# Kernel tuning notes

Measured on AMD Instinct MI355X. Metric: run time of the kernel, lower is better.

The kernel has to match this reference:

```python
import jax, jax.numpy as jnp
import numpy as np

B, SST, SL = 16, 256, 48
VOCAB, D, CH = 16384, 64, 112
TPI = 0.0


def setup_inputs() -> dict:
    key = jax.random.key(0)
    ks = jax.random.split(key, 26)
    def n(k, shp, s=0.05):
        return jax.random.normal(k, shp, dtype=jnp.float32) * s
    return {
        "x": jax.random.randint(ks[0], (B, SST), 0, VOCAB),
        "ees": n(ks[1], (B, D, SL), 1.0),
        "emb": n(ks[2], (VOCAB, D)),
        "cl0_w": n(ks[3], (CH, D, 1)),  "cl0_b": n(ks[4], (CH,)),
        "cl1_w": n(ks[5], (CH, CH, 3)), "cl1_b": n(ks[6], (CH,)),
        "claa_w": n(ks[7], (CH, CH, 3)), "claa_b": n(ks[8], (CH,)),
        "clfa_w": n(ks[9], (CH, CH, 3)), "clfa_b": n(ks[10], (CH,)),
        "ccac_w": n(ks[11], (CH, CH, 3)), "ccac_b": n(ks[12], (CH,)),
        "cib_w": n(ks[13], (D, CH, 1)),  "cib_b": n(ks[14], (D,)),
        "cpr1_w": n(ks[15], (D, 2 * D, 1)), "cpr1_b": n(ks[16], (D,)),
        "cpr2_w": n(ks[17], (D, D, 1)),  "cpr2_b": n(ks[18], (D,)),
        "cma_w": n(ks[19], (CH, D, 1)),  "cma_b": n(ks[20], (CH,)),
        "ccf_w": n(ks[21], (D, CH, 1)),  "ccf_b": n(ks[22], (D,)),
        "fff_b": n(ks[23], (VOCAB,)),
    }


def _conv1x1(x, w, b):
    # x: [B,C,S], w: [O,C,1] -> [B,O,S]
    return jnp.einsum('oc,bcs->bos', w[:, :, 0], x) + b[None, :, None]


def _conv3(x, w, b):
    # valid 1D conv, channels-first. x: [B,C,S+2] -> [B,O,S]
    y = jax.lax.conv_general_dilated(x, w, (1,), 'VALID',
                                     dimension_numbers=('NCH', 'OIH', 'NCH'))
    return y + b[None, :, None]


def _forward(x, ees, emb, cl0_w, cl0_b, cl1_w, cl1_b, claa_w, claa_b,
             clfa_w, clfa_b, ccac_w, ccac_b, cib_w, cib_b,
             cpr1_w, cpr1_b, cpr2_w, cpr2_b, cma_w, cma_b,
             ccf_w, ccf_b, fff_b):
    b = x.shape[0]
    pre_d = jnp.transpose(emb[x], (0, 2, 1))            # [B,64,SST]
    t = _conv1x1(pre_d, cl0_w, cl0_b)                   # [B,112,SST]
    tp = jnp.full((b, CH, 2), TPI, dtype=t.dtype)       # tpi pad columns

    # split cpr layer1 weight into the t-half and ees-half (concat along ch)
    wt, we = cpr1_w[:, :D, 0], cpr1_w[:, D:, 0]

    def stage(t_in, conv_w, conv_b):
        tt = jnp.concatenate([tp, t_in], axis=2)        # [B,112,SST+2]
        xconv = jax.nn.relu(_conv3(tt, conv_w, conv_b))  # [B,112,SST]
        c = _conv1x1(xconv, cib_w, cib_b)               # [B,64,SST]
        # all-pairs broadcast (sl x sst) + 1x1-conv MLP, equivalent to
        # repeat/concat/cpr in the original, without duplicating data
        h = (jnp.einsum('oc,bcs->bos', wt, c)[:, :, None, :]
             + jnp.einsum('oc,bcl->bol', we, ees)[:, :, :, None]
             + cpr1_b[None, :, None, None])             # [B,64,SL,SST]
        h = jax.nn.relu(h)
        h = jax.nn.relu(jnp.einsum('oc,bcls->bols', cpr2_w[:, :, 0], h)
                        + cpr2_b[None, :, None, None])
        m = jnp.max(h, axis=2)                          # max over sl -> [B,64,SST]
        return _conv1x1(m, cma_w, cma_b) + xconv        # residual add

    t = stage(t, cl1_w, cl1_b)
    t = stage(t, claa_w, claa_b)
    t = stage(t, clfa_w, clfa_b)
    t = stage(t, ccac_w, ccac_b)

    ccf_out = _conv1x1(t, ccf_w, ccf_b)                 # [B,64,SST]
    # tied-weight output projection: [B,SST,64] @ emb.T -> [B,SST,VOCAB]
    output = jnp.einsum('bds,vd->bsv', ccf_out, emb) + fff_b
    return output, pre_d, ccf_out


def reference(x, ees, emb, cl0_w, cl0_b, cl1_w, cl1_b, claa_w, claa_b,
              clfa_w, clfa_b, ccac_w, ccac_b, cib_w, cib_b,
              cpr1_w, cpr1_b, cpr2_w, cpr2_b, cma_w, cma_b,
              ccf_w, ccf_b, fff_b):
    return _forward(x, ees, emb, cl0_w, cl0_b, cl1_w, cl1_b, claa_w, claa_b,
                    clfa_w, clfa_b, ccac_w, ccac_b, cib_w, cib_b,
                    cpr1_w, cpr1_b, cpr2_w, cpr2_b, cma_w, cma_b,
                    ccf_w, ccf_b, fff_b)
```

## Files before the change

### kernel.cpp

```cpp
#include <hip/hip_runtime.h>

#define B_ 16
#define SST 256
#define SL 48
#define VOCAB 16384
#define D_ 64
#define CH 112

#define OUT0_ELEMS ((size_t)B_*SST*VOCAB)
#define OUT1_ELEMS (B_*D_*SST)

typedef __attribute__((ext_vector_type(8))) short s8v;
typedef __attribute__((ext_vector_type(4))) float f32x4;

#define MFMA(a,b,c) __builtin_amdgcn_mfma_f32_16x16x32_bf16(a, b, c, 0, 0, 0)

__device__ __forceinline__ void split1(float f, unsigned short* h, unsigned short* l) {
    unsigned u = __float_as_uint(f);
    *h = (unsigned short)(u >> 16);
    float lo = f - __uint_as_float(u & 0xffff0000u);
    *l = (unsigned short)(__float_as_uint(lo) >> 16);
}
__device__ __forceinline__ uint2 split_pack2(float f0, float f1) {
    unsigned u0 = __float_as_uint(f0), u1 = __float_as_uint(f1);
    unsigned hp = (u0 >> 16) | (u1 & 0xffff0000u);
    float l0 = f0 - __uint_as_float(u0 & 0xffff0000u);
    float l1 = f1 - __uint_as_float(u1 & 0xffff0000u);
    unsigned lp = (__float_as_uint(l0) >> 16) | (__float_as_uint(l1) & 0xffff0000u);
    return make_uint2(hp, lp);
}

__global__ void e_kernel(const float* __restrict__ ees,
                         const float* __restrict__ cpr1_w,
                         const float* __restrict__ cpr1_b,
                         const float* __restrict__ cib_b,
                         float* __restrict__ Eb) {
    int bl = blockIdx.x;
    int b = bl / SL, l = bl % SL;
    int tid = threadIdx.x;
    __shared__ float ec[D_];
    ec[tid] = ees[(b*D_ + tid)*SL + l];
    __syncthreads();
    const float* wrow = cpr1_w + tid*(2*D_);
    float acc = cpr1_b[tid];
    #pragma unroll
    for (int k = 0; k < D_; ++k) acc += wrow[k]*cib_b[k];
    #pragma unroll
    for (int c = 0; c < D_; ++c) acc += wrow[D_ + c]*ec[c];
    Eb[(b*SL + l)*D_ + tid] = acc;
}

__global__ void emb2bf_kernel(const float* __restrict__ emb,
                              unsigned short* __restrict__ hi,
                              unsigned short* __restrict__ lo) {
    int i = blockIdx.x*256 + threadIdx.x;
    float4 v = reinterpret_cast<const float4*>(emb)[i];
    ushort4 h, l;
    split1(v.x, &h.x, &l.x);
    split1(v.y, &h.y, &l.y);
    split1(v.z, &h.z, &l.z);
    split1(v.w, &h.w, &l.w);
    reinterpret_cast<ushort4*>(hi)[i] = h;
    reinterpret_cast<ushort4*>(lo)[i] = l;
}

__global__ void conv_prep_kernel(const float* __restrict__ w0, const float* __restrict__ w1,
                                 const float* __restrict__ w2, const float* __restrict__ w3,
                                 unsigned short* __restrict__ Wch, unsigned short* __restrict__ Wcl) {
    int gid = blockIdx.x*256 + threadIdx.x;
    int c = gid & 127;
    int o = (gid >> 7) & 127;
    int kst = gid >> 14;
    int k = kst % 3, st = kst / 3;
    const float* w = (st == 0) ? w0 : (st == 1) ? w1 : (st == 2) ? w2 : w3;
    float v = (o < CH && c < CH) ? w[o*CH*3 + c*3 + k] : 0.f;
    unsigned short h, l; split1(v, &h, &l);
    Wch[gid] = h; Wcl[gid] = l;
}

__global__ void shared_prep_kernel(const float* __restrict__ cpr1_w,
                                   const float* __restrict__ cib_w,
                                   const float* __restrict__ cpr2_w,
                                   const float* __restrict__ cma_w,
                                   const float* __restrict__ ccf_w,
                                   const float* __restrict__ cl0_w,
                                   unsigned short* __restrict__ Wcomb_h, unsigned short* __restrict__ Wcomb_l,
                                   unsigned short* __restrict__ W2h, unsigned short* __restrict__ W2l,
                                   unsigned short* __restrict__ cmah, unsigned short* __restrict__ cmal,
                                   unsigned short* __restrict__ ccfh, unsigned short* __restrict__ ccfl,
                                   unsigned short* __restrict__ cl0h, unsigned short* __restrict__ cl0l) {
    int gid = blockIdx.x*256 + threadIdx.x;
    unsigned short h, l;
    if (gid < 8192) {
        int o = gid >> 7, c = gid & 127;
        float v = 0.f;
        if (c < CH) {
            const float* wrow = cpr1_w + o*(2*D_);
            #pragma unroll
            for (int k = 0; k < D_; ++k) v += wrow[k]*cib_w[k*CH + c];
        }
        split1(v, &h, &l); Wcomb_h[gid] = h; Wcomb_l[gid] = l;
    } else if (gid < 12288) {
        int idx = gid - 8192;
        split1(cpr2_w[idx], &h, &l); W2h[idx] = h; W2l[idx] = l;
    } else if (gid < 20480) {
        int idx = gid - 12288;
        int o = idx >> 6;
        float v = (o < CH) ? cma_w[idx] : 0.f;
        split1(v, &h, &l); cmah[idx] = h; cmal[idx] = l;
    } else if (gid < 28672) {
        int idx = gid - 20480;
        int d = idx >> 7, c = idx & 127;
        float v = (c < CH) ? ccf_w[d*CH + c] : 0.f;
        split1(v, &h, &l); ccfh[idx] = h; ccfl[idx] = l;
    } else {
        int idx = gid - 28672;
        int o = idx >> 6;
        float v = (o < CH) ? cl0_w[idx] : 0.f;
        split1(v, &h, &l); cl0h[idx] = h; cl0l[idx] = l;
    }
}


__global__ __launch_bounds__(512) void f1_kernel(
    const int* __restrict__ x, const float* __restrict__ emb,
    const unsigned short* __restrict__ cl0h, const unsigned short* __restrict__ cl0l,
    const float* __restrict__ cl0_b,
    const unsigned short* __restrict__ Wch, const unsigned short* __restrict__ Wcl,
    const float* __restrict__ conv_b,
    const unsigned short* __restrict__ Wcombh, const unsigned short* __restrict__ Wcombl,
    float* __restrict__ pre_d, float* __restrict__ xc_g, float* __restrict__ ac_g) {
    int b = blockIdx.x >> 4, s0 = (blockIdx.x & 15) << 4;
    int tid = threadIdx.x, w = tid >> 6, lane = tid & 63, n = lane & 15, kg = lane >> 4;

    __shared__ unsigned short Eg_h[18*72], Eg_l[18*72];
    __shared__ unsigned short Tt_h[18*136], Tt_l[18*136];
    __shared__ unsigned short Xt_h[16*136], Xt_l[16*136];

    for (int idx = tid; idx < 288; idx += 512) {
        int si = idx >> 4, c4 = (idx & 15)*4;
        int s = s0 - 2 + si;
        float4 v = make_float4(0.f, 0.f, 0.f, 0.f);
        if (s >= 0) {
            int tok = x[b*SST + s];
            v = *reinterpret_cast<const float4*>(&emb[tok*D_ + c4]);
        }
        ushort4 h, l;
        split1(v.x, &h.x, &l.x); split1(v.y, &h.y, &l.y);
        split1(v.z, &h.z, &l.z); split1(v.w, &h.w, &l.w);
        *reinterpret_cast<ushort4*>(&Eg_h[si*72 + c4]) = h;
        *reinterpret_cast<ushort4*>(&Eg_l[si*72 + c4]) = l;
        if (si >= 2) {
            pre_d[(b*D_ + c4+0)*SST + s] = v.x;
            pre_d[(b*D_ + c4+1)*SST + s] = v.y;
            pre_d[(b*D_ + c4+2)*SST + s] = v.z;
            pre_d[(b*D_ + c4+3)*SST + s] = v.w;
        }
    }
    __syncthreads();

    int ob = w*16 + kg*4;
    #pragma unroll
    for (int ct = 0; ct < 2; ++ct) {
        int si = ct*2 + n;
        f32x4 tv = {0.f, 0.f, 0.f, 0.f};
        #pragma unroll
        for (int kt = 0; kt < 2; ++kt) {
            int cc = kt*32 + kg*8;
            s8v bh = *(const s8v*)&Eg_h[si*72 + cc];
            s8v bl = *(const s8v*)&Eg_l[si*72 + cc];
            int ai = (w*16 + n)*64 + cc;
            s8v ah = *(const s8v*)&cl0h[ai];
            s8v al = *(const s8v*)&cl0l[ai];
            tv = MFMA(ah, bh, tv); tv = MFMA(ah, bl, tv); tv = MFMA(al, bh, tv);
        }
        int s = s0 - 2 + si;
        float r0 = 0.f, r1 = 0.f, r2 = 0.f, r3 = 0.f;
        if (s >= 0) {
            r0 = tv[0] + ((ob+0 < CH) ? cl0_b[ob+0] : 0.f);
            r1 = tv[1] + ((ob+1 < CH) ? cl0_b[ob+1] : 0.f);
            r2 = tv[2] + ((ob+2 < CH) ? cl0_b[ob+2] : 0.f);
            r3 = tv[3] + ((ob+3 < CH) ? cl0_b[ob+3] : 0.f);
        }
        uint2 p01 = split_pack2(r0, r1), p23 = split_pack2(r2, r3);
        *reinterpret_cast<uint2*>(&Tt_h[si*136 + ob]) = make_uint2(p01.x, p23.x);
        *reinterpret_cast<uint2*>(&Tt_l[si*136 + ob]) = make_uint2(p01.y, p23.y);
    }
    __syncthreads();

    f32x4 xcv = {0.f, 0.f, 0.f, 0.f};
    #pragma unroll
    for (int k = 0; k < 3; ++k)
        #pragma unroll
        for (int kt = 0; kt < 4; ++kt) {
            int cc = kt*32 + kg*8;
            s8v bh = *(const s8v*)&Tt_h[(n + k)*136 + cc];
            s8v bl = *(const s8v*)&Tt_l[(n + k)*136 + cc];
            int ai = (k*128 + w*16 + n)*128 + cc;
            s8v ah = *(const s8v*)&Wch[ai];
            s8v al = *(const s8v*)&Wcl[ai];
            xcv = MFMA(ah, bh, xcv); xcv = MFMA(ah, bl, xcv); xcv = MFMA(al, bh, xcv);
        }
    #pragma unroll
    for (int r = 0; r < 4; ++r) {
        float cb = (ob + r < CH) ? conv_b[ob + r] : 0.f;
        xcv[r] = fmaxf(xcv[r] + cb, 0.f);
    }
    {
        uint2 p01 = split_pack2(xcv[0], xcv[1]), p23 = split_pack2(xcv[2], xcv[3]);
        *reinterpret_cast<uint2*>(&Xt_h[n*136 + ob]) = make_uint2(p01.x, p23.x);
        *reinterpret_cast<uint2*>(&Xt_l[n*136 + ob]) = make_uint2(p01.y, p23.y);
        *reinterpret_cast<float4*>(&xc_g[(b*SST + s0 + n)*128 + ob]) =
            make_float4(xcv[0], xcv[1], xcv[2], xcv[3]);
    }
    __syncthreads();

    if (w < 4) {
        f32x4 acc = {0.f, 0.f, 0.f, 0.f};
        #pragma unroll
        for (int kt = 0; kt < 4; ++kt) {
            int cc = kt*32 + kg*8;
            int ai = (w*16 + n)*128 + cc;
            s8v ah = *(const s8v*)&Wcombh[ai];
            s8v al = *(const s8v*)&Wcombl[ai];
            s8v bh = *(const s8v*)&Xt_h[n*136 + cc];
            s8v bl = *(const s8v*)&Xt_l[n*136 + cc];
            acc = MFMA(ah, bh, acc); acc = MFMA(ah, bl, acc); acc = MFMA(al, bh, acc);
        }
        *reinterpret_cast<float4*>(&ac_g[(b*SST + s0 + n)*64 + w*16 + kg*4]) =
            make_float4(acc[0], acc[1], acc[2], acc[3]);
    }
}

__global__ __launch_bounds__(512) void fmid_kernel(
    const unsigned short* __restrict__ Mmh, const unsigned short* __restrict__ Mml,
    const unsigned short* __restrict__ cmah, const unsigned short* __restrict__ cmal,
    const float* __restrict__ cma_b, const float* __restrict__ xc_prev,
    const unsigned short* __restrict__ Wch, const unsigned short* __restrict__ Wcl,
    const float* __restrict__ conv_b,
    const unsigned short* __restrict__ Wcombh, const unsigned short* __restrict__ Wcombl,
    float* __restrict__ xc_g, float* __restrict__ ac_g) {
    int b = blockIdx.x >> 4, s0 = (blockIdx.x & 15) << 4;
    int tid = threadIdx.x, w = tid >> 6, lane = tid & 63, n = lane & 15, kg = lane >> 4;

    __shared__ unsigned short Eg_h[18*72], Eg_l[18*72];
    __shared__ unsigned short Tt_h[18*136], Tt_l[18*136];
    __shared__ unsigned short Xt_h[16*136], Xt_l[16*136];

    for (int idx = tid; idx < 288; idx += 512) {
        int si = idx >> 4, c4 = (idx & 15)*4;
        int s = s0 - 2 + si;
        uint2 h = make_uint2(0, 0), l = make_uint2(0, 0);
        if (s >= 0) {
            h = *reinterpret_cast<const uint2*>(&Mmh[(b*SST + s)*64 + c4]);
            l = *reinterpret_cast<const uint2*>(&Mml[(b*SST + s)*64 + c4]);
        }
        *reinterpret_cast<uint2*>(&Eg_h[si*72 + c4]) = h;
        *reinterpret_cast<uint2*>(&Eg_l[si*72 + c4]) = l;
    }
    __syncthreads();

    int ob = w*16 + kg*4;
    #pragma unroll
    for (int ct = 0; ct < 2; ++ct) {
        int si = ct*2 + n;
        f32x4 tv = {0.f, 0.f, 0.f, 0.f};
        #pragma unroll
        for (int kt = 0; kt < 2; ++kt) {
            int cc = kt*32 + kg*8;
            s8v bh = *(const s8v*)&Eg_h[si*72 + cc];
            s8v bl = *(const s8v*)&Eg_l[si*72 + cc];
            int ai = (w*16 + n)*64 + cc;
            s8v ah = *(const s8v*)&cmah[ai];
            s8v al = *(const s8v*)&cmal[ai];
            tv = MFMA(ah, bh, tv); tv = MFMA(ah, bl, tv); tv = MFMA(al, bh, tv);
        }
        int s = s0 - 2 + si;
        float r0 = 0.f, r1 = 0.f, r2 = 0.f, r3 = 0.f;
        if (s >= 0) {
            float4 xr = *reinterpret_cast<const float4*>(&xc_prev[(b*SST + s)*128 + ob]);
            r0 = tv[0] + ((ob+0 < CH) ? cma_b[ob+0] : 0.f) + xr.x;
            r1 = tv[1] + ((ob+1 < CH) ? cma_b[ob+1] : 0.f) + xr.y;
            r2 = tv[2] + ((ob+2 < CH) ? cma_b[ob+2] : 0.f) + xr.z;
            r3 = tv[3] + ((ob+3 < CH) ? cma_b[ob+3] : 0.f) + xr.w;
        }
        uint2 p01 = split_pack2(r0, r1), p23 = split_pack2(r2, r3);
        *reinterpret_cast<uint2*>(&Tt_h[si*136 + ob]) = make_uint2(p01.x, p23.x);
        *reinterpret_cast<uint2*>(&Tt_l[si*136 + ob]) = make_uint2(p01.y, p23.y);
    }
    __syncthreads();

    f32x4 xcv = {0.f, 0.f, 0.f, 0.f};
    #pragma unroll
    for (int k = 0; k < 3; ++k)
        #pragma unroll
        for (int kt = 0; kt < 4; ++kt) {
            int cc = kt*32 + kg*8;
            s8v bh = *(const s8v*)&Tt_h[(n + k)*136 + cc];
            s8v bl = *(const s8v*)&Tt_l[(n + k)*136 + cc];
            int ai = (k*128 + w*16 + n)*128 + cc;
            s8v ah = *(const s8v*)&Wch[ai];
            s8v al = *(const s8v*)&Wcl[ai];
            xcv = MFMA(ah, bh, xcv); xcv = MFMA(ah, bl, xcv); xcv = MFMA(al, bh, xcv);
        }
    #pragma unroll
    for (int r = 0; r < 4; ++r) {
        float cb = (ob + r < CH) ? conv_b[ob + r] : 0.f;
        xcv[r] = fmaxf(xcv[r] + cb, 0.f);
    }
    {
        uint2 p01 = split_pack2(xcv[0], xcv[1]), p23 = split_pack2(xcv[2], xcv[3]);
        *reinterpret_cast<uint2*>(&Xt_h[n*136 + ob]) = make_uint2(p01.x, p23.x);
        *reinterpret_cast<uint2*>(&Xt_l[n*136 + ob]) = make_uint2(p01.y, p23.y);
        *reinterpret_cast<float4*>(&xc_g[(b*SST + s0 + n)*128 + ob]) =
            make_float4(xcv[0], xcv[1], xcv[2], xcv[3]);
    }
    __syncthreads();

    if (w < 4) {
        f32x4 acc = {0.f, 0.f, 0.f, 0.f};
        #pragma unroll
        for (int kt = 0; kt < 4; ++kt) {
            int cc = kt*32 + kg*8;
            int ai = (w*16 + n)*128 + cc;
            s8v ah = *(const s8v*)&Wcombh[ai];
            s8v al = *(const s8v*)&Wcombl[ai];
            s8v bh = *(const s8v*)&Xt_h[n*136 + cc];
            s8v bl = *(const s8v*)&Xt_l[n*136 + cc];
            acc = MFMA(ah, bh, acc); acc = MFMA(ah, bl, acc); acc = MFMA(al, bh, acc);
        }
        *reinterpret_cast<float4*>(&ac_g[(b*SST + s0 + n)*64 + w*16 + kg*4]) =
            make_float4(acc[0], acc[1], acc[2], acc[3]);
    }
}

__global__ __launch_bounds__(256) void h2max_kernel(
    const float* __restrict__ ac_g, const float* __restrict__ Eb,
    const unsigned short* __restrict__ W2h, const unsigned short* __restrict__ W2l,
    const float* __restrict__ cpr2_b,
    unsigned short* __restrict__ Mmh, unsigned short* __restrict__ Mml) {
    int b = blockIdx.x >> 6;
    int s_local = (blockIdx.x & 63)*4 + (threadIdx.x >> 6);
    int lane = threadIdx.x & 63, n = lane & 15, kg = lane >> 4;
    int bs = b*SST + s_local;

    __shared__ float El[48*68];
    for (int idx = threadIdx.x; idx < 768; idx += 256) {
        int l = idx >> 4, c4 = (idx & 15)*4;
        *reinterpret_cast<float4*>(&El[l*68 + c4]) =
            *reinterpret_cast<const float4*>(&Eb[(b*SL + l)*64 + c4]);
    }

    const float* ap = ac_g + bs*64;
    float4 a00 = *reinterpret_cast<const float4*>(ap + kg*8);
    float4 a01 = *reinterpret_cast<const float4*>(ap + kg*8 + 4);
    float4 a10 = *reinterpret_cast<const float4*>(ap + 32 + kg*8);
    float4 a11 = *reinterpret_cast<const float4*>(ap + 32 + kg*8 + 4);

    s8v a2h[4][2];
    #pragma unroll
    for (int mt = 0; mt < 4; ++mt)
        #pragma unroll
        for (int kt = 0; kt < 2; ++kt)
            a2h[mt][kt] = *(const s8v*)&W2h[(mt*16 + n)*64 + kt*32 + kg*8];

    int o_lane = ((n >> 2) << 4) + (kg << 2) + (n & 3);
    float b2_lane = cpr2_b[o_lane];
    __syncthreads();

    f32x4 acc[4][3];
    #pragma unroll
    for (int mt = 0; mt < 4; ++mt)
        #pragma unroll
        for (int lt = 0; lt < 3; ++lt)
            acc[mt][lt] = (f32x4){0.f, 0.f, 0.f, 0.f};

    #pragma unroll
    for (int kt = 0; kt < 2; ++kt) {
        int cc = kt*32 + kg*8;
        float4 aA = (kt == 0) ? a00 : a10;
        float4 aB = (kt == 0) ? a01 : a11;
        s8v a2l[4];
        #pragma unroll
        for (int mt = 0; mt < 4; ++mt)
            a2l[mt] = *(const s8v*)&W2l[(mt*16 + n)*64 + cc];
        #pragma unroll
        for (int lt = 0; lt < 3; ++lt) {
            const float* ep = &El[(lt*16 + n)*68 + cc];
            float4 e0 = *reinterpret_cast<const float4*>(ep);
            float4 e1 = *reinterpret_cast<const float4*>(ep + 4);
            float h0 = fmaxf(aA.x + e0.x, 0.f);
            float h1 = fmaxf(aA.y + e0.y, 0.f);
            float h2 = fmaxf(aA.z + e0.z, 0.f);
            float h3 = fmaxf(aA.w + e0.w, 0.f);
            float h4 = fmaxf(aB.x + e1.x, 0.f);
            float h5 = fmaxf(aB.y + e1.y, 0.f);
            float h6 = fmaxf(aB.z + e1.z, 0.f);
            float h7 = fmaxf(aB.w + e1.w, 0.f);
            uint2 q0 = split_pack2(h0, h1);
            uint2 q1 = split_pack2(h2, h3);
            uint2 q2 = split_pack2(h4, h5);
            uint2 q3 = split_pack2(h6, h7);
            union { unsigned u[4]; s8v v; } Bh, Bl;
            Bh.u[0] = q0.x; Bh.u[1] = q1.x; Bh.u[2] = q2.x; Bh.u[3] = q3.x;
            Bl.u[0] = q0.y; Bl.u[1] = q1.y; Bl.u[2] = q2.y; Bl.u[3] = q3.y;
            #pragma unroll
            for (int mt = 0; mt < 4; ++mt) {
                acc[mt][lt] = MFMA(a2h[mt][kt], Bh.v, acc[mt][lt]);
                acc[mt][lt] = MFMA(a2h[mt][kt], Bl.v, acc[mt][lt]);
                acc[mt][lt] = MFMA(a2l[mt], Bh.v, acc[mt][lt]);
            }
        }
    }

    float mx[16];
    #pragma unroll
    for (int mt = 0; mt < 4; ++mt)
        #pragma unroll
        for (int r = 0; r < 4; ++r)
            mx[mt*4 + r] = fmaxf(fmaxf(acc[mt][0][r], acc[mt][1][r]), acc[mt][2][r]);
    #pragma unroll
    for (int step = 0; step < 4; ++step) {
        int msk = 1 << step;
        #pragma unroll
        for (int i = 0; i < 16; ++i)
            mx[i] = fmaxf(mx[i], __shfl_xor(mx[i], msk));
    }
    float sel = mx[0];
    #pragma unroll
    for (int i = 1; i < 16; ++i)
        sel = (n == i) ? mx[i] : sel;
    float mval = fmaxf(sel + b2_lane, 0.f);
    unsigned short mh, ml; split1(mval, &mh, &ml);
    Mmh[bs*64 + o_lane] = mh;
    Mml[bs*64 + o_lane] = ml;
}

__global__ __launch_bounds__(256) void cmaccf_kernel(
    const unsigned short* __restrict__ Mmh, const unsigned short* __restrict__ Mml,
    const unsigned short* __restrict__ cmah, const unsigned short* __restrict__ cmal,
    const float* __restrict__ cma_b, const float* __restrict__ xc_prev,
    const unsigned short* __restrict__ ccfh, const unsigned short* __restrict__ ccfl,
    const float* __restrict__ ccf_b,
    float* __restrict__ ccf_out,
    unsigned short* __restrict__ Ahi, unsigned short* __restrict__ Alo) {
    int b = blockIdx.x >> 4, s0 = (blockIdx.x & 15) << 4;
    int tid = threadIdx.x, w = tid >> 6, lane = tid & 63, n = lane & 15, kg = lane >> 4;

    __shared__ unsigned short Mh[16*72], Ml[16*72];
    __shared__ unsigned short Th[16*136], Tl[16*136];

    for (int idx = tid; idx < 256; idx += 256) {
        int s = idx >> 4, c4 = (idx & 15)*4;
        *reinterpret_cast<uint2*>(&Mh[s*72 + c4]) =
            *reinterpret_cast<const uint2*>(&Mmh[(b*SST + s0 + s)*64 + c4]);
        *reinterpret_cast<uint2*>(&Ml[s*72 + c4]) =
            *reinterpret_cast<const uint2*>(&Mml[(b*SST + s0 + s)*64 + c4]);
    }
    __syncthreads();

    #pragma unroll
    for (int half = 0; half < 2; ++half) {
        int ob = (half*4 + w)*16 + kg*4;
        f32x4 tv = {0.f, 0.f, 0.f, 0.f};
        #pragma unroll
        for (int kt = 0; kt < 2; ++kt) {
            int cc = kt*32 + kg*8;
            s8v bh = *(const s8v*)&Mh[n*72 + cc];
            s8v bl = *(const s8v*)&Ml[n*72 + cc];
            int ai = ((half*4 + w)*16 + n)*64 + cc;
            s8v ah = *(const s8v*)&cmah[ai];
            s8v al = *(const s8v*)&cmal[ai];
            tv = MFMA(ah, bh, tv); tv = MFMA(ah, bl, tv); tv = MFMA(al, bh, tv);
        }
        int s = s0 + n;
        float4 xr = *reinterpret_cast<const float4*>(&xc_prev[(b*SST + s)*128 + ob]);
        float r0 = tv[0] + ((ob+0 < CH) ? cma_b[ob+0] : 0.f) + xr.x;
        float r1 = tv[1] + ((ob+1 < CH) ? cma_b[ob+1] : 0.f) + xr.y;
        float r2 = tv[2] + ((ob+2 < CH) ? cma_b[ob+2] : 0.f) + xr.z;
        float r3 = tv[3] + ((ob+3 < CH) ? cma_b[ob+3] : 0.f) + xr.w;
        uint2 p01 = split_pack2(r0, r1), p23 = split_pack2(r2, r3);
        *reinterpret_cast<uint2*>(&Th[n*136 + ob]) = make_uint2(p01.x, p23.x);
        *reinterpret_cast<uint2*>(&Tl[n*136 + ob]) = make_uint2(p01.y, p23.y);
    }
    __syncthreads();

    f32x4 acc = {0.f, 0.f, 0.f, 0.f};
    #pragma unroll
    for (int kt = 0; kt < 4; ++kt) {
        int cc = kt*32 + kg*8;
        int ai = (w*16 + n)*128 + cc;
        s8v ah = *(const s8v*)&ccfh[ai];
        s8v al = *(const s8v*)&ccfl[ai];
        s8v bh = *(const s8v*)&Th[n*136 + cc];
        s8v bl = *(const s8v*)&Tl[n*136 + cc];
        acc = MFMA(ah, bh, acc); acc = MFMA(ah, bl, acc); acc = MFMA(al, bh, acc);
    }
    int d0 = w*16 + kg*4, s = s0 + n;
    float v0 = acc[0] + ccf_b[d0+0];
    float v1 = acc[1] + ccf_b[d0+1];
    float v2 = acc[2] + ccf_b[d0+2];
    float v3 = acc[3] + ccf_b[d0+3];
    ccf_out[(b*D_ + d0+0)*SST + s] = v0;
    ccf_out[(b*D_ + d0+1)*SST + s] = v1;
    ccf_out[(b*D_ + d0+2)*SST + s] = v2;
    ccf_out[(b*D_ + d0+3)*SST + s] = v3;
    uint2 p01 = split_pack2(v0, v1), p23 = split_pack2(v2, v3);
    *reinterpret_cast<uint2*>(&Ahi[(b*SST + s)*64 + d0]) = make_uint2(p01.x, p23.x);
    *reinterpret_cast<uint2*>(&Alo[(b*SST + s)*64 + d0]) = make_uint2(p01.y, p23.y);
}

__global__ __launch_bounds__(256) void logits_mfma_kernel(
    const unsigned short* __restrict__ Ahi,
    const unsigned short* __restrict__ Alo,
    const unsigned short* __restrict__ Bhi,
    const unsigned short* __restrict__ Blo,
    const float* __restrict__ fffb,
    float* __restrict__ out) {
    int ntile = blockIdx.x & 127;
    int mtile = blockIdx.x >> 7;
    int wid = threadIdx.x >> 6;
    int lane = threadIdx.x & 63;
    int wm = wid >> 1, wn = wid & 1;
    int m0 = mtile*128 + wm*64;
    int v0 = ntile*128 + wn*64;
    int row16 = lane & 15, kg = lane >> 4;

    const short* Ah = (const short*)Ahi;
    const short* Al = (const short*)Alo;
    const short* Bh = (const short*)Bhi;
    const short* Bl = (const short*)Blo;

    f32x4 acc[4][4];
    #pragma unroll
    for (int mi = 0; mi < 4; ++mi)
        #pragma unroll
        for (int ni = 0; ni < 4; ++ni)
            acc[mi][ni] = (f32x4){0.f, 0.f, 0.f, 0.f};

    #pragma unroll
    for (int kk = 0; kk < 2; ++kk) {
        int koff = kk*32 + kg*8;
        s8v ah[4], al[4], bh[4], bl[4];
        #pragma unroll
        for (int mi = 0; mi < 4; ++mi) {
            int r = (m0 + mi*16 + row16)*D_ + koff;
            ah[mi] = *reinterpret_cast<const s8v*>(Ah + r);
            al[mi] = *reinterpret_cast<const s8v*>(Al + r);
        }
        #pragma unroll
        for (int ni = 0; ni < 4; ++ni) {
            int r = (v0 + ni*16 + row16)*D_ + koff;
            bh[ni] = *reinterpret_cast<const s8v*>(Bh + r);
            bl[ni] = *reinterpret_cast<const s8v*>(Bl + r);
        }
        #pragma unroll
        for (int mi = 0; mi < 4; ++mi)
            #pragma unroll
            for (int ni = 0; ni < 4; ++ni) {
                acc[mi][ni] = MFMA(ah[mi], bh[ni], acc[mi][ni]);
                acc[mi][ni] = MFMA(ah[mi], bl[ni], acc[mi][ni]);
                acc[mi][ni] = MFMA(al[mi], bh[ni], acc[mi][ni]);
            }
    }

    #pragma unroll
    for (int ni = 0; ni < 4; ++ni) {
        int v = v0 + ni*16 + row16;
        float fb = fffb[v];
        #pragma unroll
        for (int mi = 0; mi < 4; ++mi) {
            int mbase = m0 + mi*16 + kg*4;
            #pragma unroll
            for (int r = 0; r < 4; ++r) {
                __builtin_nontemporal_store(acc[mi][ni][r] + fb,
                    &out[(size_t)(mbase + r)*VOCAB + v]);
            }
        }
    }
}

extern "C" void kernel_launch(void* const* d_in, const int* in_sizes, int n_in,
                              void* d_out, int out_size, void* d_ws, size_t ws_size,
                              hipStream_t stream) {
    const int*   x     = (const int*)d_in[0];
    const float* ees   = (const float*)d_in[1];
    const float* emb   = (const float*)d_in[2];
    const float* cl0_w = (const float*)d_in[3];
    const float* cl0_b = (const float*)d_in[4];
    const float* cl1_w = (const float*)d_in[5];
    const float* cl1_b = (const float*)d_in[6];
    const float* claa_w= (const float*)d_in[7];
    const float* claa_b= (const float*)d_in[8];
    const float* clfa_w= (const float*)d_in[9];
    const float* clfa_b= (const float*)d_in[10];
    const float* ccac_w= (const float*)d_in[11];
    const float* ccac_b= (const float*)d_in[12];
    const float* cib_w = (const float*)d_in[13];
    const float* cib_b = (const float*)d_in[14];
    const float* cpr1_w= (const float*)d_in[15];
    const float* cpr1_b= (const float*)d_in[16];
    const float* cpr2_w= (const float*)d_in[17];
    const float* cpr2_b= (const float*)d_in[18];
    const float* cma_w = (const float*)d_in[19];
    const float* cma_b = (const float*)d_in[20];
    const float* ccf_w = (const float*)d_in[21];
    const float* ccf_b = (const float*)d_in[22];
    const float* fff_b = (const float*)d_in[23];

    float* out = (float*)d_out;
    float* out_pre = out + OUT0_ELEMS;
    float* out_ccf = out_pre + OUT1_ELEMS;

    unsigned short* EmbHi = (unsigned short*)d_ws;
    unsigned short* EmbLo = EmbHi + VOCAB*D_;
    unsigned short* Ahi   = EmbLo + VOCAB*D_;
    unsigned short* Alo   = Ahi + B_*SST*D_;

    char* sc = (char*)d_out + (size_t)16*1024*1024;
    float*          Eb    = (float*)sc;            sc += B_*SL*D_*4;
    unsigned short* Wch   = (unsigned short*)sc;   sc += 4*3*128*128*2;
    unsigned short* Wcl   = (unsigned short*)sc;   sc += 4*3*128*128*2;
    unsigned short* Wcombh= (unsigned short*)sc;   sc += 64*128*2;
    unsigned short* Wcombl= (unsigned short*)sc;   sc += 64*128*2;
    unsigned short* W2h   = (unsigned short*)sc;   sc += 64*64*2;
    unsigned short* W2l   = (unsigned short*)sc;   sc += 64*64*2;
    unsigned short* cmah  = (unsigned short*)sc;   sc += 128*64*2;
    unsigned short* cmal  = (unsigned short*)sc;   sc += 128*64*2;
    unsigned short* ccfh  = (unsigned short*)sc;   sc += 64*128*2;
    unsigned short* ccfl  = (unsigned short*)sc;   sc += 64*128*2;
    unsigned short* cl0h  = (unsigned short*)sc;   sc += 128*64*2;
    unsigned short* cl0l  = (unsigned short*)sc;   sc += 128*64*2;
    float*          xc_a  = (float*)sc;            sc += (size_t)B_*SST*128*4;
    float*          xc_b  = (float*)sc;            sc += (size_t)B_*SST*128*4;
    float*          ac_g  = (float*)sc;            sc += (size_t)B_*SST*64*4;
    unsigned short* Mmh   = (unsigned short*)sc;   sc += B_*SST*64*2;
    unsigned short* Mml   = (unsigned short*)sc;   sc += B_*SST*64*2;

    conv_prep_kernel<<<768, 256, 0, stream>>>(cl1_w, claa_w, clfa_w, ccac_w, Wch, Wcl);
    shared_prep_kernel<<<144, 256, 0, stream>>>(cpr1_w, cib_w, cpr2_w, cma_w, ccf_w, cl0_w,
        Wcombh, Wcombl, W2h, W2l, cmah, cmal, ccfh, ccfl, cl0h, cl0l);
    emb2bf_kernel<<<VOCAB*D_/4/256, 256, 0, stream>>>(emb, EmbHi, EmbLo);
    e_kernel<<<B_*SL, 64, 0, stream>>>(ees, cpr1_w, cpr1_b, cib_b, Eb);

    const int WCS = 3*128*128;
    f1_kernel<<<256, 512, 0, stream>>>(x, emb, cl0h, cl0l, cl0_b,
        Wch + 0*WCS, Wcl + 0*WCS, cl1_b, Wcombh, Wcombl, out_pre, xc_a, ac_g);
    h2max_kernel<<<1024, 256, 0, stream>>>(ac_g, Eb, W2h, W2l, cpr2_b, Mmh, Mml);
    fmid_kernel<<<256, 512, 0, stream>>>(Mmh, Mml, cmah, cmal, cma_b, xc_a,
        Wch + 1*WCS, Wcl + 1*WCS, claa_b, Wcombh, Wcombl, xc_b, ac_g);
    h2max_kernel<<<1024, 256, 0, stream>>>(ac_g, Eb, W2h, W2l, cpr2_b, Mmh, Mml);
    fmid_kernel<<<256, 512, 0, stream>>>(Mmh, Mml, cmah, cmal, cma_b, xc_b,
        Wch + 2*WCS, Wcl + 2*WCS, clfa_b, Wcombh, Wcombl, xc_a, ac_g);
    h2max_kernel<<<1024, 256, 0, stream>>>(ac_g, Eb, W2h, W2l, cpr2_b, Mmh, Mml);
    fmid_kernel<<<256, 512, 0, stream>>>(Mmh, Mml, cmah, cmal, cma_b, xc_a,
        Wch + 3*WCS, Wcl + 3*WCS, ccac_b, Wcombh, Wcombl, xc_b, ac_g);
    h2max_kernel<<<1024, 256, 0, stream>>>(ac_g, Eb, W2h, W2l, cpr2_b, Mmh, Mml);

    cmaccf_kernel<<<256, 256, 0, stream>>>(Mmh, Mml, cmah, cmal, cma_b, xc_b,
        ccfh, ccfl, ccf_b, out_ccf, Ahi, Alo);
    logits_mfma_kernel<<<(B_*SST/128)*(VOCAB/128), 256, 0, stream>>>(
        Ahi, Alo, EmbHi, EmbLo, fff_b, out);
}
```

Before: 203.9 us.

## Transpose logits MFMA operands to emit vectorized float4 output stores

Restructures the logits GEMM so the embedding rows are the MFMA A operand and the activations the B operand. Each lane then holds four consecutive vocab entries and can write them with one 16-byte nontemporal store instead of four scalar stores. The tiling also changes to 32 rows by 1024 vocab per 512-thread block, with each wave owning 128 vocab columns. The goal is to cut store instruction count and improve write coalescing on the 268 MB output, at the cost of a different register footprint and more embedding reads per block.

```diff
diff --git a/kernel.cpp b/kernel.cpp
--- a/kernel.cpp
+++ b/kernel.cpp
@@ -120,7 +120,6 @@
         split1(v, &h, &l); cl0h[idx] = h; cl0l[idx] = l;
     }
 }
-
 
 __global__ __launch_bounds__(512) void f1_kernel(
     const int* __restrict__ x, const float* __restrict__ emb,
@@ -510,72 +509,72 @@
     *reinterpret_cast<uint2*>(&Alo[(b*SST + s)*64 + d0]) = make_uint2(p01.y, p23.y);
 }
 
-__global__ __launch_bounds__(256) void logits_mfma_kernel(
+__global__ __launch_bounds__(512) void logits_mfma_kernel(
     const unsigned short* __restrict__ Ahi,
     const unsigned short* __restrict__ Alo,
     const unsigned short* __restrict__ Bhi,
     const unsigned short* __restrict__ Blo,
     const float* __restrict__ fffb,
     float* __restrict__ out) {
-    int ntile = blockIdx.x & 127;
-    int mtile = blockIdx.x >> 7;
-    int wid = threadIdx.x >> 6;
-    int lane = threadIdx.x & 63;
-    int wm = wid >> 1, wn = wid & 1;
-    int m0 = mtile*128 + wm*64;
-    int v0 = ntile*128 + wn*64;
-    int row16 = lane & 15, kg = lane >> 4;
-
-    const short* Ah = (const short*)Ahi;
-    const short* Al = (const short*)Alo;
-    const short* Bh = (const short*)Bhi;
-    const short* Bl = (const short*)Blo;
-
-    f32x4 acc[4][4];
-    #pragma unroll
-    for (int mi = 0; mi < 4; ++mi)
-        #pragma unroll
-        for (int ni = 0; ni < 4; ++ni)
-            acc[mi][ni] = (f32x4){0.f, 0.f, 0.f, 0.f};
+    int mtile = blockIdx.x & 127;
+    int vtile = blockIdx.x >> 7;
+    int wv = threadIdx.x >> 6;
+    int lane = threadIdx.x & 63, n = lane & 15, kg = lane >> 4;
+    int m0 = mtile*32;
+    int v0 = vtile*1024 + wv*128;
+
+    const short* Ch = (const short*)Ahi;
+    const short* Cl = (const short*)Alo;
+    const short* Eh = (const short*)Bhi;
+    const short* El = (const short*)Blo;
+
+    f32x4 acc[2][8];
+    #pragma unroll
+    for (int mi = 0; mi < 2; ++mi)
+        #pragma unroll
+        for (int vi = 0; vi < 8; ++vi)
+            acc[mi][vi] = (f32x4){0.f, 0.f, 0.f, 0.f};
 
     #pragma unroll
     for (int kk = 0; kk < 2; ++kk) {
         int koff = kk*32 + kg*8;
-        s8v ah[4], al[4], bh[4], bl[4];
-        #pragma unroll
-        for (int mi = 0; mi < 4; ++mi) {
-            int r = (m0 + mi*16 + row16)*D_ + koff;
-            ah[mi] = *reinterpret_cast<const s8v*>(Ah + r);
-            al[mi] = *reinterpret_cast<const s8v*>(Al + r);
-        }
-        #pragma unroll
-        for (int ni = 0; ni < 4; ++ni) {
-            int r = (v0 + ni*16 + row16)*D_ + koff;
-            bh[ni] = *reinterpret_cast<const s8v*>(Bh + r);
-            bl[ni] = *reinterpret_cast<const s8v*>(Bl + r);
-        }
-        #pragma unroll
-        for (int mi = 0; mi < 4; ++mi)
+        s8v eh[8], el[8], ch[2], cl[2];
+        #pragma unroll
+        for (int vi = 0; vi < 8; ++vi) {
+            int r = (v0 + vi*16 + n)*D_ + koff;
+            eh[vi] = *reinterpret_cast<const s8v*>(Eh + r);
+            el[vi] = *reinterpret_cast<const s8v*>(El + r);
+        }
+        #pragma unroll
+        for (int mi = 0; mi < 2; ++mi) {
+            int r = (m0 + mi*16 + n)*D_ + koff;
+            ch[mi] = *reinterpret_cast<const s8v*>(Ch + r);
+            cl[mi] = *reinterpret_cast<const s8v*>(Cl + r);
+        }
+        #pragma unroll
+        for (int mi = 0; mi < 2; ++mi)
             #pragma unroll
-            for (int ni = 0; ni < 4; ++ni) {
-                acc[mi][ni] = MFMA(ah[mi], bh[ni], acc[mi][ni]);
-                acc[mi][ni] = MFMA(ah[mi], bl[ni], acc[mi][ni]);
-                acc[mi][ni] = MFMA(al[mi], bh[ni], acc[mi][ni]);
+            for (int vi = 0; vi < 8; ++vi) {
+                acc[mi][vi] = MFMA(eh[vi], ch[mi], acc[mi][vi]);
+                acc[mi][vi] = MFMA(eh[vi], cl[mi], acc[mi][vi]);
+                acc[mi][vi] = MFMA(el[vi], ch[mi], acc[mi][vi]);
             }
     }
 
     #pragma unroll
-    for (int ni = 0; ni < 4; ++ni) {
-        int v = v0 + ni*16 + row16;
-        float fb = fffb[v];
-        #pragma unroll
-        for (int mi = 0; mi < 4; ++mi) {
-            int mbase = m0 + mi*16 + kg*4;
-            #pragma unroll
-            for (int r = 0; r < 4; ++r) {
-                __builtin_nontemporal_store(acc[mi][ni][r] + fb,
-                    &out[(size_t)(mbase + r)*VOCAB + v]);
-            }
+    for (int vi = 0; vi < 8; ++vi) {
+        int vbase = v0 + vi*16 + kg*4;
+        float4 fb = *reinterpret_cast<const float4*>(&fffb[vbase]);
+        #pragma unroll
+        for (int mi = 0; mi < 2; ++mi) {
+            int m = m0 + mi*16 + n;
+            f32x4 o4;
+            o4[0] = acc[mi][vi][0] + fb.x;
+            o4[1] = acc[mi][vi][1] + fb.y;
+            o4[2] = acc[mi][vi][2] + fb.z;
+            o4[3] = acc[mi][vi][3] + fb.w;
+            __builtin_nontemporal_store(o4,
+                reinterpret_cast<f32x4*>(&out[(size_t)m*VOCAB + vbase]));
         }
     }
 }
@@ -659,6 +658,6 @@
 
     cmaccf_kernel<<<256, 256, 0, stream>>>(Mmh, Mml, cmah, cmal, cma_b, xc_b,
         ccfh, ccfl, ccf_b, out_ccf, Ahi, Alo);
-    logits_mfma_kernel<<<(B_*SST/128)*(VOCAB/128), 256, 0, stream>>>(
+    logits_mfma_kernel<<<16*128, 512, 0, stream>>>(
         Ahi, Alo, EmbHi, EmbLo, fff_b, out);
 }
```

Result: slower. 278.4 us (+36.6%).
